# Performance work log

Hardware: AMD Instinct MI355X
Metric: run time of the kernel (lower is better)

The kernel has to match this reference:

```python
import jax, jax.numpy as jnp
import numpy as np
from jax import lax

B, C_IN, C_OUT, KK, KS = 8, 32, 64, 4, 3
D, H, W = 32, 64, 64
PAD = 1

def setup_inputs() -> dict:
    key = jax.random.key(0)
    ks = jax.random.split(key, 12)
    s = 0.02
    return {
        "x": jax.random.normal(ks[0], (B, C_IN, D, H, W), jnp.float32),
        # K candidate conv kernels and biases
        "weight": jax.random.normal(ks[1], (KK, C_OUT, C_IN, KS, KS, KS), jnp.float32) * s,
        "cbias": jnp.zeros((KK, C_OUT), jnp.float32),
        "temperature": jnp.float32(34.0),
        # attention key path: BN(affine, eval-mode) -> GELU -> 1x1 conv (linear)
        "bn1_g": jnp.ones((C_IN,), jnp.float32),
        "bn1_b": jnp.zeros((C_IN,), jnp.float32),
        "w1": jax.random.normal(ks[2], (C_IN, C_IN), jnp.float32) * s,
        "b1": jnp.zeros((C_IN,), jnp.float32),
        "bn2_g": jnp.ones((C_IN,), jnp.float32),
        "bn2_b": jnp.zeros((C_IN,), jnp.float32),
        "w2": jax.random.normal(ks[3], (C_IN, C_IN), jnp.float32) * s,
        "b2": jnp.zeros((C_IN,), jnp.float32),
        "bn3_g": jnp.ones((C_IN,), jnp.float32),
        "bn3_b": jnp.zeros((C_IN,), jnp.float32),
        "w3": jax.random.normal(ks[4], (KK, C_IN), jnp.float32) * s,
        "b3": jnp.zeros((KK,), jnp.float32),
    }

def _attention(p, temperature, bn1_g, bn1_b, w1, b1, bn2_g, bn2_b, w2, b2, bn3_g, bn3_b, w3, b3):
    # p: [B, C] pooled features. 1x1x1 convs on 1x1x1 maps == linear layers.
    gelu = lambda t: jax.nn.gelu(t, approximate=False)  # torch nn.GELU default is erf
    a = gelu(p * bn1_g + bn1_b)          # BN (eval: rm=0, rv=1) + GELU
    a = a @ w1.T + b1
    a = gelu(a * bn2_g + bn2_b)
    a = a @ w2.T + b2
    a = a + p                            # ResidualLayer (plain add)
    a = a * bn3_g + bn3_b
    logits = a @ w3.T + b3               # [B, K]
    return jax.nn.softmax(logits / temperature, axis=1)

def reference(x, weight, cbias, temperature, bn1_g, bn1_b, w1, b1,
              bn2_g, bn2_b, w2, b2, bn3_g, bn3_b, w3, b3):
    # x: [B, C_in, D, H, W]
    p = x.mean(axis=(2, 3, 4))  # AdaptiveAvgPool3d(1)
    attn = _attention(p, temperature, bn1_g, bn1_b, w1, b1,
                      bn2_g, bn2_b, w2, b2, bn3_g, bn3_b, w3, b3)  # [B, K]
    # per-sample aggregated kernels / bias
    agg_w = jnp.einsum('bk,koidhw->boidhw', attn, weight)  # [B, O, I, k, k, k]
    agg_b = attn @ cbias                                    # [B, O]
    # grouped-conv trick (groups=B) == per-sample conv3d -> vmap over batch
    def conv1(xi, wi):
        return lax.conv_general_dilated(
            xi[None], wi, window_strides=(1, 1, 1),
            padding=[(PAD, PAD)] * 3,
            dimension_numbers=('NCDHW', 'OIDHW', 'NCDHW'))[0]
    out = jax.vmap(conv1)(x, agg_w)  # [B, O, D, H, W]
    return out + agg_b[:, :, None, None, None]
```

## Files before the change

kernel.cpp:

```cpp
#include <hip/hip_runtime.h>
#include <hip/hip_bf16.h>
#include <math.h>

#define B_   8
#define CIN  32
#define COUT 64
#define KK_  4
#define DD   32
#define HH   64
#define WW   64
#define HW   (HH*WW)
#define DHW  (DD*HH*WW)

typedef __attribute__((ext_vector_type(8)))  short bf16x8;
typedef __attribute__((ext_vector_type(16))) float f32x16;

__device__ __forceinline__ unsigned short f2bf(float f) {
    union { float f; unsigned int u; } v; v.f = f;
    return (unsigned short)((v.u + 0x7FFFu + ((v.u >> 16) & 1u)) >> 16);
}
__device__ __forceinline__ void gll16(const void* g, void* l) {
    __builtin_amdgcn_global_load_lds(
        (const __attribute__((address_space(1))) void*)g,
        (__attribute__((address_space(3))) void*)l, 16, 0, 0);
}

__global__ __launch_bounds__(256) void transpose_kernel(const float* __restrict__ x,
                                                        unsigned short* __restrict__ xt,
                                                        float* __restrict__ pblk) {
    const int t = threadIdx.x;
    const int r = t >> 6, w = t & 63;
    const int hb = blockIdx.x;
    const int h = (hb << 2) + r;
    const int d = blockIdx.y, b = blockIdx.z;

    const float* xb = x + (size_t)b*CIN*DHW + (size_t)d*HW + (size_t)h*WW + w;
    float f[CIN];
    #pragma unroll
    for (int c = 0; c < CIN; ++c) f[c] = xb[(size_t)c * DHW];

    unsigned int packed[CIN/2];
    #pragma unroll
    for (int c2 = 0; c2 < CIN/2; ++c2) {
        unsigned int lo = f2bf(f[2*c2]);
        unsigned int hi = f2bf(f[2*c2+1]);
        packed[c2] = lo | (hi << 16);
    }
    char* row = (char*)xt + (size_t)((b*DD + d)*HH + h) * 4096;
    #pragma unroll
    for (int q = 0; q < 4; ++q) {
        uint4 v = make_uint4(packed[4*q], packed[4*q+1], packed[4*q+2], packed[4*q+3]);
        *(uint4*)(row + q*1024 + (((w << 4)) ^ (q << 4))) = v;
    }

    #pragma unroll
    for (int off = 32; off > 0; off >>= 1) {
        #pragma unroll
        for (int c = 0; c < CIN; ++c) f[c] += __shfl_xor(f[c], off);
    }
    __shared__ float ws4[4][CIN];
    if ((t & 63) < CIN) ws4[r][t & 63] = f[t & 63];
    __syncthreads();
    if (t < CIN)
        pblk[(size_t)((b*DD + d)*16 + hb)*CIN + t] =
            ws4[0][t] + ws4[1][t] + ws4[2][t] + ws4[3][t];
}

__device__ __forceinline__ float gelu_erf(float v) {
    return 0.5f * v * (1.f + erff(v * 0.70710678118654752f));
}

__global__ void attn_kernel(const float* __restrict__ pblk,
                            const float* __restrict__ temperature,
                            const float* __restrict__ bn1_g, const float* __restrict__ bn1_b,
                            const float* __restrict__ w1,    const float* __restrict__ b1,
                            const float* __restrict__ bn2_g, const float* __restrict__ bn2_b,
                            const float* __restrict__ w2,    const float* __restrict__ b2,
                            const float* __restrict__ bn3_g, const float* __restrict__ bn3_b,
                            const float* __restrict__ w3,    const float* __restrict__ b3,
                            const float* __restrict__ cbias,
                            float* __restrict__ attn_out, float* __restrict__ aggb_out) {
    __shared__ float A[B_][CIN], A2[B_][CIN];
    __shared__ float L[B_][KK_], ATT[B_][KK_];
    const int t = threadIdx.x;
    const int b = t >> 5, c = t & 31;

    float pv = 0.f;
    for (int i = 0; i < DD*16; ++i) pv += pblk[(size_t)(b*DD*16 + i)*CIN + c];
    pv *= (1.f / (float)DHW);

    A[b][c] = gelu_erf(pv * bn1_g[c] + bn1_b[c]);
    __syncthreads();

    float s = b1[c];
    for (int j = 0; j < CIN; ++j) s += A[b][j] * w1[c*CIN + j];
    A2[b][c] = gelu_erf(s * bn2_g[c] + bn2_b[c]);
    __syncthreads();

    float s2 = b2[c];
    for (int j = 0; j < CIN; ++j) s2 += A2[b][j] * w2[c*CIN + j];
    s2 += pv;
    s2 = s2 * bn3_g[c] + bn3_b[c];
    __syncthreads();
    A[b][c] = s2;
    __syncthreads();

    if (c < KK_) {
        float lv = b3[c];
        for (int j = 0; j < CIN; ++j) lv += A[b][j] * w3[c*CIN + j];
        L[b][c] = lv;
    }
    __syncthreads();

    const float T = temperature[0];
    if (c < KK_) {
        float m = fmaxf(fmaxf(L[b][0], L[b][1]), fmaxf(L[b][2], L[b][3]));
        float e = expf((L[b][c] - m) / T);
        float den = 0.f;
        for (int j = 0; j < KK_; ++j) den += expf((L[b][j] - m) / T);
        float av = e / den;
        ATT[b][c] = av;
        attn_out[b*KK_ + c] = av;
    }
    __syncthreads();

    for (int o = c; o < COUT; o += CIN) {
        float sb = 0.f;
        for (int k = 0; k < KK_; ++k) sb += ATT[b][k] * cbias[k*COUT + o];
        aggb_out[b*COUT + o] = sb;
    }
}

__global__ void aggw_kernel(const float* __restrict__ weight,
                            const float* __restrict__ attn,
                            unsigned short* __restrict__ wt) {
    const int idx = blockIdx.x * 256 + threadIdx.x;
    const int ci   = idx & 31;
    const int co   = (idx >> 5) & 63;
    int r          = idx >> 11;
    const int kpos = r % 27;
    const int b    = r / 27;
    float s = 0.f;
    #pragma unroll
    for (int k = 0; k < KK_; ++k)
        s += attn[b*KK_ + k] * weight[((k*COUT + co)*CIN + ci)*27 + kpos];
    wt[idx] = f2bf(s);
}

__global__ __launch_bounds__(256, 2) void conv_mfma(const unsigned short* __restrict__ xt,
                                                    const unsigned short* __restrict__ wt,
                                                    const float* __restrict__ aggb,
                                                    float* __restrict__ out) {
    __shared__ char smem[19 * 4096];
    const int t    = threadIdx.x;
    const int lane = t & 63;
    const int wid  = t >> 6;
    const int cv   = wid >> 1;
    const int wv   = wid & 1;
    const int lw   = lane & 31, lh = lane >> 5;

    const int id = blockIdx.x;
    const int b  = id & 7;
    const int h  = (id >> 3) & 63;
    const int d0 = ((id >> 9) & 7) << 2;

    const char* xb  = (const char*)xt + (size_t)(b*DD)*HH*4096;
    const char* wtb = (const char*)wt + (size_t)b * 27 * 4096 + (cv << 11);

    *(uint4*)&smem[18*4096 + t*16] = make_uint4(0u,0u,0u,0u);

    auto stage_row = [&](int j, int ho) {
        const int zd = d0 - 1 + j, yh = h - 1 + ho;
        char* dst = smem + (size_t)((j*3 + ho) << 12);
        if ((unsigned)zd < DD && (unsigned)yh < HH) {
            const char* src = xb + ((size_t)(zd*HH + yh) << 12) + lane*16;
            #pragma unroll
            for (int q = 0; q < 4; ++q) gll16(src + (q << 10), dst + (q << 10));
        } else {
            #pragma unroll
            for (int q = 0; q < 4; ++q)
                *(uint4*)(dst + (q << 10) + lane*16) = make_uint4(0u,0u,0u,0u);
        }
    };
    for (int rid = wid; rid < 18; rid += 4)
        stage_row(rid / 3, rid % 3);
    __syncthreads();

    f32x16 binit;
    #pragma unroll
    for (int reg = 0; reg < 16; ++reg)
        binit[reg] = aggb[b*COUT + (cv << 5) + (reg & 3) + ((reg >> 2) << 3) + (lh << 2)];

    f32x16 acc[4];
    #pragma unroll
    for (int r = 0; r < 4; ++r) acc[r] = binit;

    const int a_off = lw*64 + lh*16;
    const int o0 = lh, o1 = 2 + lh;
    const int ZR = 18*4096;

    #pragma unroll
    for (int kh = 0; kh < 3; ++kh) {
        bf16x8 av[9][2];
        #pragma unroll
        for (int kd = 0; kd < 3; ++kd)
            #pragma unroll
            for (int kw = 0; kw < 3; ++kw) {
                const char* wk = wtb + (size_t)(((kd*3 + kh)*3 + kw) << 12);
                av[kd*3 + kw][0] = *(const bf16x8*)(wk + a_off);
                av[kd*3 + kw][1] = *(const bf16x8*)(wk + 32 + a_off);
            }

        #pragma unroll
        for (int kw = 0; kw < 3; ++kw) {
            const int wp  = (wv << 5) + lw + kw - 1;
            const bool oob = ((unsigned)wp >= (unsigned)WW);
            const int wpc = oob ? lw : wp;
            const int sw0 = (o0 << 10) + ((wpc << 4) ^ (o0 << 4));
            const int sw1 = (o1 << 10) + ((wpc << 4) ^ (o1 << 4));

            bf16x8 bc[6][2];
            #pragma unroll
            for (int j = 0; j < 6; ++j) {
                const int base = oob ? ZR : ((j*3 + kh) << 12);
                bc[j][0] = *(const bf16x8*)&smem[base + sw0];
                bc[j][1] = *(const bf16x8*)&smem[base + sw1];
            }

            __builtin_amdgcn_s_setprio(1);
            #pragma unroll
            for (int khalf = 0; khalf < 2; ++khalf) {
                #pragma unroll
                for (int kd = 0; kd < 3; ++kd) {
                    #pragma unroll
                    for (int r = 0; r < 4; ++r) {
                        const int j = r + kd;
                        acc[r] = __builtin_amdgcn_mfma_f32_32x32x16_bf16(
                            av[kd*3 + kw][khalf], bc[j][khalf], acc[r], 0, 0, 0);
                    }
                }
            }
            __builtin_amdgcn_s_setprio(0);
        }
    }

    const int sp0 = h*WW + (wv << 5) + lw;
    #pragma unroll
    for (int reg = 0; reg < 16; ++reg) {
        const int co = (cv << 5) + (reg & 3) + ((reg >> 2) << 3) + (lh << 2);
        float* oc = out + ((size_t)(b*COUT + co))*DHW + sp0;
        #pragma unroll
        for (int r = 0; r < 4; ++r)
            oc[(size_t)(d0 + r)*HW] = acc[r][reg];
    }
}

extern "C" void kernel_launch(void* const* d_in, const int* in_sizes, int n_in,
                              void* d_out, int out_size, void* d_ws, size_t ws_size,
                              hipStream_t stream) {
    const float* x           = (const float*)d_in[0];
    const float* weight      = (const float*)d_in[1];
    const float* cbias       = (const float*)d_in[2];
    const float* temperature = (const float*)d_in[3];
    const float* bn1_g       = (const float*)d_in[4];
    const float* bn1_b       = (const float*)d_in[5];
    const float* w1          = (const float*)d_in[6];
    const float* b1          = (const float*)d_in[7];
    const float* bn2_g       = (const float*)d_in[8];
    const float* bn2_b       = (const float*)d_in[9];
    const float* w2          = (const float*)d_in[10];
    const float* b2          = (const float*)d_in[11];
    const float* bn3_g       = (const float*)d_in[12];
    const float* bn3_b       = (const float*)d_in[13];
    const float* w3          = (const float*)d_in[14];
    const float* b3          = (const float*)d_in[15];
    float* out = (float*)d_out;

    char* ws = (char*)d_ws;
    float*          attn = (float*)(ws + 1024);
    float*          aggb = (float*)(ws + 4096);
    float*          pblk = (float*)(ws + 65536);
    unsigned short* wt   = (unsigned short*)(ws + 622592);
    unsigned short* xt   = (unsigned short*)(ws + 1507328);

    transpose_kernel<<<dim3(HH/4, DD, B_), 256, 0, stream>>>(x, xt, pblk);
    attn_kernel<<<1, 256, 0, stream>>>(pblk, temperature,
                                       bn1_g, bn1_b, w1, b1,
                                       bn2_g, bn2_b, w2, b2,
                                       bn3_g, bn3_b, w3, b3,
                                       cbias, attn, aggb);
    aggw_kernel<<<(B_*27*COUT*CIN)/256, 256, 0, stream>>>(weight, attn, wt);
    conv_mfma<<<dim3(4096), 256, 0, stream>>>(xt, wt, aggb, out);
}
```

Before: 190.9 us.

## Make conv a persistent-style block streaming depth slices through a ring buffer

The conv kernel now runs 256 blocks of 512 threads. Each block covers two adjacent H rows for one batch and loops over all 8 depth chunks, keeping a 10-slot ring buffer of input rows in 160KB of LDS. The next depth rows are prefetched asynchronously while the current chunk's MFMAs run. This overlaps loads with compute and reuses overlapping halo rows across both depth and H. The trade-off is only 256 blocks on a GPU with many CUs, so occupancy is low and load balance is coarse. Out-of-bounds W is now handled by selecting zero instead of using a zero LDS row.

```diff
diff --git a/kernel.cpp b/kernel.cpp
--- a/kernel.cpp
+++ b/kernel.cpp
@@ -147,31 +147,31 @@
     wt[idx] = f2bf(s);
 }
 
-__global__ __launch_bounds__(256, 2) void conv_mfma(const unsigned short* __restrict__ xt,
+__global__ __launch_bounds__(512, 2) void conv_mfma(const unsigned short* __restrict__ xt,
                                                     const unsigned short* __restrict__ wt,
                                                     const float* __restrict__ aggb,
                                                     float* __restrict__ out) {
-    __shared__ char smem[19 * 4096];
+    __shared__ char smem[163840];
     const int t    = threadIdx.x;
     const int lane = t & 63;
     const int wid  = t >> 6;
-    const int cv   = wid >> 1;
-    const int wv   = wid & 1;
+    const int hv   = wid & 1;
+    const int wv   = (wid >> 1) & 1;
+    const int cv   = wid >> 2;
     const int lw   = lane & 31, lh = lane >> 5;
 
     const int id = blockIdx.x;
     const int b  = id & 7;
-    const int h  = (id >> 3) & 63;
-    const int d0 = ((id >> 9) & 7) << 2;
+    const int hp = id >> 3;
+    const int h  = (hp << 1) + hv;
 
     const char* xb  = (const char*)xt + (size_t)(b*DD)*HH*4096;
     const char* wtb = (const char*)wt + (size_t)b * 27 * 4096 + (cv << 11);
 
-    *(uint4*)&smem[18*4096 + t*16] = make_uint4(0u,0u,0u,0u);
-
-    auto stage_row = [&](int j, int ho) {
-        const int zd = d0 - 1 + j, yh = h - 1 + ho;
-        char* dst = smem + (size_t)((j*3 + ho) << 12);
+    auto stage_row = [&](int zd, int ho) {
+        const int slot = (zd + 40) % 10;
+        char* dst = smem + slot*16384 + (ho << 12);
+        const int yh = (hp << 1) - 1 + ho;
         if ((unsigned)zd < DD && (unsigned)yh < HH) {
             const char* src = xb + ((size_t)(zd*HH + yh) << 12) + lane*16;
             #pragma unroll
@@ -182,8 +182,12 @@
                 *(uint4*)(dst + (q << 10) + lane*16) = make_uint4(0u,0u,0u,0u);
         }
     };
-    for (int rid = wid; rid < 18; rid += 4)
-        stage_row(rid / 3, rid % 3);
+
+    #pragma unroll
+    for (int i = 0; i < 3; ++i) {
+        const int rid = wid*3 + i;
+        stage_row((rid >> 2) - 1, rid & 3);
+    }
     __syncthreads();
 
     f32x16 binit;
@@ -197,61 +201,83 @@
 
     const int a_off = lw*64 + lh*16;
     const int o0 = lh, o1 = 2 + lh;
-    const int ZR = 18*4096;
-
-    #pragma unroll
-    for (int kh = 0; kh < 3; ++kh) {
-        bf16x8 av[9][2];
-        #pragma unroll
-        for (int kd = 0; kd < 3; ++kd)
+    const bf16x8 bz = {};
+
+    for (int s = 0; s < 8; ++s) {
+        const int d0 = s << 2;
+        if (s < 7) {
+            #pragma unroll
+            for (int i = 0; i < 2; ++i) {
+                const int rid = wid*2 + i;
+                stage_row(d0 + 5 + (rid >> 2), rid & 3);
+            }
+        }
+        int rbj[6];
+        #pragma unroll
+        for (int j = 0; j < 6; ++j) rbj[j] = ((d0 - 1 + j + 40) % 10) * 16384;
+
+        #pragma unroll
+        for (int kh = 0; kh < 3; ++kh) {
+            const int rowb = (hv + kh) << 12;
+            bf16x8 av[9][2];
+            #pragma unroll
+            for (int kd = 0; kd < 3; ++kd)
+                #pragma unroll
+                for (int kw = 0; kw < 3; ++kw) {
+                    const char* wk = wtb + (size_t)(((kd*3 + kh)*3 + kw) << 12);
+                    av[kd*3 + kw][0] = *(const bf16x8*)(wk + a_off);
+                    av[kd*3 + kw][1] = *(const bf16x8*)(wk + 32 + a_off);
+                }
+
             #pragma unroll
             for (int kw = 0; kw < 3; ++kw) {
-                const char* wk = wtb + (size_t)(((kd*3 + kh)*3 + kw) << 12);
-                av[kd*3 + kw][0] = *(const bf16x8*)(wk + a_off);
-                av[kd*3 + kw][1] = *(const bf16x8*)(wk + 32 + a_off);
-            }
-
-        #pragma unroll
-        for (int kw = 0; kw < 3; ++kw) {
-            const int wp  = (wv << 5) + lw + kw - 1;
-            const bool oob = ((unsigned)wp >= (unsigned)WW);
-            const int wpc = oob ? lw : wp;
-            const int sw0 = (o0 << 10) + ((wpc << 4) ^ (o0 << 4));
-            const int sw1 = (o1 << 10) + ((wpc << 4) ^ (o1 << 4));
-
-            bf16x8 bc[6][2];
-            #pragma unroll
-            for (int j = 0; j < 6; ++j) {
-                const int base = oob ? ZR : ((j*3 + kh) << 12);
-                bc[j][0] = *(const bf16x8*)&smem[base + sw0];
-                bc[j][1] = *(const bf16x8*)&smem[base + sw1];
-            }
-
-            __builtin_amdgcn_s_setprio(1);
-            #pragma unroll
-            for (int khalf = 0; khalf < 2; ++khalf) {
+                const int wp  = (wv << 5) + lw + kw - 1;
+                const bool oob = ((unsigned)wp >= (unsigned)WW);
+                const int wpc = oob ? ((wp < 0) ? 0 : (WW - 1)) : wp;
+                const int sw0 = (o0 << 10) + ((wpc << 4) ^ (o0 << 4));
+                const int sw1 = (o1 << 10) + ((wpc << 4) ^ (o1 << 4));
+
+                bf16x8 bc[6][2];
                 #pragma unroll
-                for (int kd = 0; kd < 3; ++kd) {
+                for (int j = 0; j < 6; ++j) {
+                    bf16x8 v0 = *(const bf16x8*)&smem[rbj[j] + rowb + sw0];
+                    bf16x8 v1 = *(const bf16x8*)&smem[rbj[j] + rowb + sw1];
+                    bc[j][0] = oob ? bz : v0;
+                    bc[j][1] = oob ? bz : v1;
+                }
+
+                __builtin_amdgcn_s_setprio(1);
+                #pragma unroll
+                for (int kf = 0; kf < 2; ++kf) {
                     #pragma unroll
-                    for (int r = 0; r < 4; ++r) {
-                        const int j = r + kd;
-                        acc[r] = __builtin_amdgcn_mfma_f32_32x32x16_bf16(
-                            av[kd*3 + kw][khalf], bc[j][khalf], acc[r], 0, 0, 0);
+                    for (int kd = 0; kd < 3; ++kd) {
+                        #pragma unroll
+                        for (int r = 0; r < 4; ++r) {
+                            acc[r] = __builtin_amdgcn_mfma_f32_32x32x16_bf16(
+                                av[kd*3 + kw][kf], bc[r + kd][kf], acc[r], 0, 0, 0);
+                        }
                     }
                 }
+                __builtin_amdgcn_s_setprio(0);
             }
-            __builtin_amdgcn_s_setprio(0);
-        }
-    }
-
-    const int sp0 = h*WW + (wv << 5) + lw;
-    #pragma unroll
-    for (int reg = 0; reg < 16; ++reg) {
-        const int co = (cv << 5) + (reg & 3) + ((reg >> 2) << 3) + (lh << 2);
-        float* oc = out + ((size_t)(b*COUT + co))*DHW + sp0;
-        #pragma unroll
-        for (int r = 0; r < 4; ++r)
-            oc[(size_t)(d0 + r)*HW] = acc[r][reg];
+        }
+
+        if (s < 7) {
+            asm volatile("s_waitcnt vmcnt(0) lgkmcnt(0)" ::: "memory");
+            __builtin_amdgcn_s_barrier();
+        }
+
+        const int sp0 = h*WW + (wv << 5) + lw;
+        #pragma unroll
+        for (int reg = 0; reg < 16; ++reg) {
+            const int co = (cv << 5) + (reg & 3) + ((reg >> 2) << 3) + (lh << 2);
+            float* oc = out + ((size_t)(b*COUT + co))*DHW + sp0;
+            #pragma unroll
+            for (int r = 0; r < 4; ++r)
+                oc[(size_t)(d0 + r)*HW] = acc[r][reg];
+        }
+        #pragma unroll
+        for (int r = 0; r < 4; ++r) acc[r] = binit;
     }
 }
 
@@ -290,5 +316,5 @@
                                        bn3_g, bn3_b, w3, b3,
                                        cbias, attn, aggb);
     aggw_kernel<<<(B_*27*COUT*CIN)/256, 256, 0, stream>>>(weight, attn, wt);
-    conv_mfma<<<dim3(4096), 256, 0, stream>>>(xt, wt, aggb, out);
-}
+    conv_mfma<<<dim3(256), 512, 0, stream>>>(xt, wt, aggb, out);
+}
```

Result: slower. 444.4 us (+132.8%).
